# Kernel tuning notes

Hardware: AMD Instinct MI355X
Metric: run time of the kernel (lower is better)

The kernel has to match this reference:

```python
import jax, jax.numpy as jnp
import numpy as np

# static module config (matches init_kwargs)
DIM = 128
HEADS = 8
DW, HW, WW = 5, 7, 7  # depth/height/width window


def _neighbor_indices(D, H, W):
    """Flat circular-neighborhood indices, shape (P, n) with P=D*H*W, n=DW*HW*WW."""
    od = np.arange(DW) - (DW - 1) // 2
    oh = np.arange(HW) - (HW - 1) // 2
    ow = np.arange(WW) - (WW - 1) // 2
    dd = (np.arange(D)[:, None] + od[None, :]) % D   # (D, DW)
    hh = (np.arange(H)[:, None] + oh[None, :]) % H   # (H, HW)
    ww = (np.arange(W)[:, None] + ow[None, :]) % W   # (W, WW)
    idx = (dd[:, None, None, :, None, None] * (H * W)
           + hh[None, :, None, None, :, None] * W
           + ww[None, None, :, None, None, :])        # (D,H,W,DW,HW,WW)
    return jnp.asarray(idx.reshape(D * H * W, DW * HW * WW), dtype=jnp.int32)


def setup_inputs() -> dict:
    key = jax.random.key(0)
    k1, k2, k3, k4, k5 = jax.random.split(key, 5)
    B, D, H, W, C = 1, 5, 24, 48, DIM
    w_scale = 1.0 / np.sqrt(C)  # keep attention logits in a sane range
    return {
        "x": jax.random.normal(k1, (B, D, H, W, C), dtype=jnp.float32),
        "qkv_w": jax.random.normal(k2, (3 * C, C), dtype=jnp.float32) * w_scale,
        "qkv_b": jax.random.normal(k3, (3 * C,), dtype=jnp.float32) * 0.01,
        "proj_w": jax.random.normal(k4, (C, C), dtype=jnp.float32) * w_scale,
        "proj_b": jax.random.normal(k5, (C,), dtype=jnp.float32) * 0.01,
    }


def reference(x, qkv_w, qkv_b, proj_w, proj_b):
    B, D, H, W, C = x.shape
    P = D * H * W
    n = DW * HW * WW
    hd = C // HEADS
    scale = hd ** -0.5
    idx = _neighbor_indices(D, H, W)                      # (P, n) int32, static

    xf = x.reshape(B, P, C)
    qkv = xf @ qkv_w.T + qkv_b                            # (B, P, 3C)
    q, k, v = jnp.split(qkv, 3, axis=-1)

    q = q.reshape(B, P, HEADS, hd)                        # center-pixel query
    k_g = k[:, idx].reshape(B, P, n, HEADS, hd)           # gathered circular neighborhood
    v_g = v[:, idx].reshape(B, P, n, HEADS, hd)

    scores = jnp.einsum('bphd,bpnhd->bhpn', q, k_g) * scale
    attn = jax.nn.softmax(scores, axis=-1)                # softmax over 245 neighbors
    out = jnp.einsum('bhpn,bpnhd->bphd', attn, v_g).reshape(B, P, C)
    out = out @ proj_w.T + proj_b
    return out.reshape(B, D, H, W, C)
```

## Files before the change

kernel.cpp:

```cpp
#include <hip/hip_runtime.h>
#include <hip/hip_bf16.h>
#include <cstddef>

#define DIMC   128
#define NHEADS 8
#define HDIM   16
#define DD     5
#define HH     24
#define WW_    48
#define NPOS   (DD * HH * WW_)
#define SCALE  0.25f

typedef short  bf16x8 __attribute__((ext_vector_type(8)));
typedef float  f32x4  __attribute__((ext_vector_type(4)));

__device__ __forceinline__ unsigned short f2bf(float f) {
    unsigned u = __float_as_uint(f);
    u = (u + 0x7FFFu + ((u >> 16) & 1u)) >> 16;
    return (unsigned short)u;
}
__device__ __forceinline__ float bf2f(unsigned short s) {
    return __uint_as_float(((unsigned)s) << 16);
}

__global__ __launch_bounds__(256) void prep_kernel(
    const float* __restrict__ x,
    const float* __restrict__ wq,
    const float* __restrict__ wp,
    unsigned short* __restrict__ Axq,
    unsigned short* __restrict__ Bxq,
    unsigned short* __restrict__ Bxp)
{
    const int i = blockIdx.x * 256 + threadIdx.x;
    const bool isA = (i < 184320);
    const float* src; unsigned short* dst; int rel;
    if (isA)             { src = x;  dst = Axq; rel = i; }
    else if (i < 196608) { src = wq; dst = Bxq; rel = i - 184320; }
    else                 { src = wp; dst = Bxp; rel = i - 196608; }
    const int row = rel >> 5;
    const int c4  = rel & 31;
    const float4 v = *(const float4*)(src + (size_t)row * 128 + c4 * 4);
    ushort4 hi, lo;
    hi.x = f2bf(v.x); hi.y = f2bf(v.y); hi.z = f2bf(v.z); hi.w = f2bf(v.w);
    lo.x = f2bf(v.x - bf2f(hi.x));
    lo.y = f2bf(v.y - bf2f(hi.y));
    lo.z = f2bf(v.z - bf2f(hi.z));
    lo.w = f2bf(v.w - bf2f(hi.w));
    unsigned short* p = dst + (size_t)row * 384 + c4 * 4;
    if (isA) {
        *(ushort4*)(p)       = hi;
        *(ushort4*)(p + 128) = lo;
        *(ushort4*)(p + 256) = hi;
    } else {
        *(ushort4*)(p)       = hi;
        *(ushort4*)(p + 128) = hi;
        *(ushort4*)(p + 256) = lo;
    }
}

template <int MI, int EPI>
__global__ __launch_bounds__(256, 3) void gemm_mfma_kernel(
    const unsigned short* __restrict__ Ax,
    const unsigned short* __restrict__ Bx,
    const float* __restrict__ bias,
    float* __restrict__ C, int ldc,
    unsigned short* __restrict__ Qhl,
    unsigned short* __restrict__ Kbf,
    unsigned short* __restrict__ Vbf)
{
    __shared__ __align__(16) unsigned short Bs[64][392];

    const int tid = threadIdx.x;
    const int bn  = blockIdx.x * 64;
    const int bm  = blockIdx.y * 64 * MI;

    for (int i = tid; i < 64 * 48; i += 256) {
        const int r = i / 48, s = i % 48;
        *(ulonglong2*)(&Bs[r][s * 8]) =
            *(const ulonglong2*)(Bx + (size_t)(bn + r) * 384 + s * 8);
    }
    __syncthreads();

    const int w    = tid >> 6;
    const int lane = tid & 63;
    const int ln   = lane & 15;
    const int quad = lane >> 4;

    f32x4 acc[MI][4] = {};
    const unsigned short* arow[MI];
    #pragma unroll
    for (int mi = 0; mi < MI; ++mi)
        arow[mi] = Ax + (size_t)(bm + w * 16 * MI + mi * 16 + ln) * 384 + quad * 8;

    #pragma unroll
    for (int kc = 0; kc < 12; ++kc) {
        bf16x8 a[MI];
        #pragma unroll
        for (int mi = 0; mi < MI; ++mi) a[mi] = *(const bf16x8*)(arow[mi] + kc * 32);
        #pragma unroll
        for (int nt = 0; nt < 4; ++nt) {
            const bf16x8 b = *(const bf16x8*)(&Bs[nt * 16 + ln][kc * 32 + quad * 8]);
            #pragma unroll
            for (int mi = 0; mi < MI; ++mi)
                acc[mi][nt] = __builtin_amdgcn_mfma_f32_16x16x32_bf16(a[mi], b, acc[mi][nt], 0, 0, 0);
        }
    }

    #pragma unroll
    for (int mi = 0; mi < MI; ++mi)
        #pragma unroll
        for (int nt = 0; nt < 4; ++nt) {
            const int col = bn + nt * 16 + ln;
            const float bv = bias[col];
            #pragma unroll
            for (int r = 0; r < 4; ++r) {
                const int row = bm + w * 16 * MI + mi * 16 + quad * 4 + r;
                const float val = acc[mi][nt][r] + bv;
                if (EPI == 0) {
                    C[(size_t)row * ldc + col] = val;
                } else {
                    if (col < 128) {
                        const int h = col >> 4, ci = col & 15;
                        const unsigned short hi = f2bf(val);
                        Qhl[(size_t)row * 256 + h * 32 + ci]      = hi;
                        Qhl[(size_t)row * 256 + h * 32 + 16 + ci] = f2bf(val - bf2f(hi));
                    } else if (col < 256) {
                        Kbf[(size_t)row * 128 + (col - 128)] = f2bf(val);
                    } else {
                        Vbf[(size_t)row * 128 + (col - 256)] = f2bf(val);
                    }
                }
            }
        }
}

__global__ __launch_bounds__(256, 3) void attn_kernel(
    const unsigned short* __restrict__ Qhl,
    const unsigned short* __restrict__ Kbf,
    const unsigned short* __restrict__ Vbf,
    unsigned short* __restrict__ Ap)
{
    __shared__ __align__(16) char smem[34560];
    unsigned short (*Vt)[520] = (unsigned short(*)[520])smem;
    unsigned short (*Qb)[40]  = (unsigned short(*)[40])(smem + 16640);
    unsigned short* PwBase    = (unsigned short*)(smem + 23040);
    float* red_l              = (float*)(smem + 33280);
    float* redO               = (float*)smem;

    const int tile = blockIdx.x;
    const int h    = blockIdx.y;
    const int ty0  = (tile / 12) * 4;
    const int tx0  = (tile % 12) * 4;
    const int tid  = threadIdx.x;

    for (int i = tid; i < 1024; i += 256) {
        const int u = i >> 1, half = i & 1;
        if (u < 500) {
            const int dp = u / 100;
            const int rr = u - dp * 100;
            const int yy = rr / 10;
            const int xx = rr - yy * 10;
            int y = ty0 - 3 + yy; if (y < 0) y += HH;  if (y >= HH) y -= HH;
            int x = tx0 - 3 + xx; if (x < 0) x += WW_; if (x >= WW_) x -= WW_;
            const int g = (dp * HH + y) * WW_ + x;
            const bf16x8 v = *(const bf16x8*)(Vbf + (size_t)g * 128 + h * 16 + half * 8);
            #pragma unroll
            for (int c = 0; c < 8; ++c) Vt[half * 8 + c][u] = (unsigned short)v[c];
        } else {
            #pragma unroll
            for (int c = 0; c < 8; ++c) Vt[half * 8 + c][u] = 0;
        }
    }
    for (int i = tid; i < 320; i += 256) {
        const int p = i >> 2, seg = i & 3;
        const int d = p >> 4, s = p & 15;
        const int sy = s >> 2, sx = s & 3;
        const int g = (d * HH + ty0 + sy) * WW_ + tx0 + sx;
        *(bf16x8*)(&Qb[p][seg * 8]) = *(const bf16x8*)(Qhl + (size_t)g * 256 + h * 32 + seg * 8);
    }
    __syncthreads();

    const int w    = tid >> 6;
    const int lane = tid & 63;
    const int ln   = lane & 15;
    const int quad = lane >> 4;
    const int sy   = ln >> 2, sx = ln & 3;

    unsigned short* Pw = PwBase + w * 1280;

    bf16x8 qf[5];
    #pragma unroll
    for (int mt = 0; mt < 5; ++mt)
        qf[mt] = *(const bf16x8*)(&Qb[mt * 16 + ln][quad * 8]);

    f32x4 Ow[5] = {};
    float lsum[5] = {};

    for (int chunk = 0; chunk < 4; ++chunk) {
        const int u0 = (w * 4 + chunk) * 32;

        int rowa, rowb;
        {
            const int ua = u0 + ln      < 500 ? u0 + ln      : 499;
            const int ub = u0 + 16 + ln < 500 ? u0 + 16 + ln : 499;
            int dp = ua / 100, rr = ua - dp * 100, yy = rr / 10, xx = rr - yy * 10;
            int y = ty0 - 3 + yy; if (y < 0) y += HH;  if (y >= HH) y -= HH;
            int x = tx0 - 3 + xx; if (x < 0) x += WW_; if (x >= WW_) x -= WW_;
            rowa = (dp * HH + y) * WW_ + x;
            dp = ub / 100; rr = ub - dp * 100; yy = rr / 10; xx = rr - yy * 10;
            y = ty0 - 3 + yy; if (y < 0) y += HH;  if (y >= HH) y -= HH;
            x = tx0 - 3 + xx; if (x < 0) x += WW_; if (x >= WW_) x -= WW_;
            rowb = (dp * HH + y) * WW_ + x;
        }
        const bf16x8 ka = *(const bf16x8*)(Kbf + (size_t)rowa * 128 + h * 16 + (quad & 1) * 8);
        const bf16x8 kb = *(const bf16x8*)(Kbf + (size_t)rowb * 128 + h * 16 + (quad & 1) * 8);

        bool msk[2][4];
        #pragma unroll
        for (int b = 0; b < 2; ++b)
            #pragma unroll
            for (int r = 0; r < 4; ++r) {
                const int u = u0 + 16 * b + 4 * quad + r;
                const int rr = u % 100;
                const int uy = rr / 10, ux = rr - uy * 10;
                msk[b][r] = (u < 500) && ((unsigned)(uy - sy) <= 6u)
                                      && ((unsigned)(ux - sx) <= 6u);
            }

        const bf16x8 vf = *(const bf16x8*)(&Vt[ln][u0 + quad * 8]);

        #pragma unroll
        for (int mt = 0; mt < 5; ++mt) {
            f32x4 s0 = __builtin_amdgcn_mfma_f32_16x16x32_bf16(
                ka, qf[mt], (f32x4){0.f, 0.f, 0.f, 0.f}, 0, 0, 0);
            f32x4 s1 = __builtin_amdgcn_mfma_f32_16x16x32_bf16(
                kb, qf[mt], (f32x4){0.f, 0.f, 0.f, 0.f}, 0, 0, 0);

            unsigned short* pw = Pw + (mt & 1) * 640 + ln * 40;
            #pragma unroll
            for (int b = 0; b < 2; ++b) {
                const f32x4 s = b ? s1 : s0;
                unsigned short e[4];
                #pragma unroll
                for (int r = 0; r < 4; ++r) {
                    const float ev = msk[b][r] ? __expf(fmaf(s[r], SCALE, -8.0f)) : 0.f;
                    e[r] = f2bf(ev);
                    lsum[mt] += bf2f(e[r]);
                }
                *(unsigned*)(pw + 16 * b + 4 * quad)     = (unsigned)e[0] | ((unsigned)e[1] << 16);
                *(unsigned*)(pw + 16 * b + 4 * quad + 2) = (unsigned)e[2] | ((unsigned)e[3] << 16);
            }
            const bf16x8 pf = *(const bf16x8*)(Pw + (mt & 1) * 640 + ln * 40 + quad * 8);
            Ow[mt] = __builtin_amdgcn_mfma_f32_16x16x32_bf16(vf, pf, Ow[mt], 0, 0, 0);
        }
    }

    #pragma unroll
    for (int mt = 0; mt < 5; ++mt) {
        lsum[mt] += __shfl_xor(lsum[mt], 16);
        lsum[mt] += __shfl_xor(lsum[mt], 32);
    }

    __syncthreads();

    if (quad == 0) {
        #pragma unroll
        for (int mt = 0; mt < 5; ++mt) red_l[w * 80 + mt * 16 + ln] = lsum[mt];
    }
    #pragma unroll
    for (int mt = 0; mt < 5; ++mt)
        #pragma unroll
        for (int r = 0; r < 4; ++r)
            redO[(size_t)((w * 5 + mt) * 16 + quad * 4 + r) * 16 + ln] = Ow[mt][r];
    __syncthreads();

    for (int i = tid; i < 1280; i += 256) {
        const int m = i >> 4, c = i & 15;
        const int mt = m >> 4, mloc = m & 15;
        float o = 0.f, l = 0.f;
        #pragma unroll
        for (int w4 = 0; w4 < 4; ++w4) {
            o += redO[(size_t)((w4 * 5 + mt) * 16 + c) * 16 + mloc];
            l += red_l[w4 * 80 + m];
        }
        const float val = o / l;
        const int qsy = (mloc >> 2), qsx = mloc & 3;
        const size_t g = (size_t)((mt * HH + ty0 + qsy) * WW_ + (tx0 + qsx));
        const unsigned short hi = f2bf(val);
        const unsigned short lo = f2bf(val - bf2f(hi));
        unsigned short* row = Ap + g * 384 + h * HDIM + c;
        row[0]   = hi;
        row[128] = lo;
        row[256] = hi;
    }
}

extern "C" void kernel_launch(void* const* d_in, const int* in_sizes, int n_in,
                              void* d_out, int out_size, void* d_ws, size_t ws_size,
                              hipStream_t stream)
{
    const float* x      = (const float*)d_in[0];
    const float* qkv_w  = (const float*)d_in[1];
    const float* qkv_b  = (const float*)d_in[2];
    const float* proj_w = (const float*)d_in[3];
    const float* proj_b = (const float*)d_in[4];
    float* out = (float*)d_out;

    char* ws = (char*)d_ws;
    unsigned short* Axq = (unsigned short*)ws;  ws += (size_t)NPOS * 384 * 2;
    unsigned short* Ap  = (unsigned short*)ws;  ws += (size_t)NPOS * 384 * 2;
    unsigned short* Bxq = (unsigned short*)ws;  ws += (size_t)384 * 384 * 2;
    unsigned short* Bxp = (unsigned short*)ws;  ws += (size_t)128 * 384 * 2;
    unsigned short* Qhl = (unsigned short*)ws;  ws += (size_t)NPOS * 256 * 2;
    unsigned short* Kbf = (unsigned short*)ws;  ws += (size_t)NPOS * 128 * 2;
    unsigned short* Vbf = (unsigned short*)ws;  ws += (size_t)NPOS * 128 * 2;

    prep_kernel<<<784, 256, 0, stream>>>(x, qkv_w, proj_w, Axq, Bxq, Bxp);

    {
        dim3 grid(384 / 64, NPOS / 128);
        gemm_mfma_kernel<2, 1><<<grid, 256, 0, stream>>>(
            Axq, Bxq, qkv_b, nullptr, 0, Qhl, Kbf, Vbf);
    }
    {
        dim3 grid(72, NHEADS);
        attn_kernel<<<grid, 256, 0, stream>>>(Qhl, Kbf, Vbf, Ap);
    }
    {
        dim3 grid(DIMC / 64, NPOS / 64);
        gemm_mfma_kernel<1, 0><<<grid, 256, 0, stream>>>(
            Ap, Bxp, proj_b, out, DIMC, nullptr, nullptr, nullptr);
    }
}
```

Baseline: 107.4 us.

## Repartition attention work so each wave owns one depth slice's queries

The attention kernel now uses 320 threads (5 waves), and each wave owns the 16 queries of one depth slice and loops over all 500 neighbor keys. Previously the 4 waves split the keys and held all 5 query tiles, so partial outputs had to be reduced across waves in shared memory. The change removes that reduction and its barriers and moves neighbor row indices and per-query mask bitmasks into shared-memory tables. It also switches to exp2 with folded constants, truncates to bf16 instead of rounding, and packs two V rows per shared store. The trade-off is fewer blocks per CU and more serial MFMA work per wave.

```diff
diff --git a/kernel.cpp b/kernel.cpp
--- a/kernel.cpp
+++ b/kernel.cpp
@@ -134,18 +134,17 @@
         }
 }
 
-__global__ __launch_bounds__(256, 3) void attn_kernel(
+__global__ __launch_bounds__(320, 2) void attn_kernel(
     const unsigned short* __restrict__ Qhl,
     const unsigned short* __restrict__ Kbf,
     const unsigned short* __restrict__ Vbf,
     unsigned short* __restrict__ Ap)
 {
-    __shared__ __align__(16) char smem[34560];
-    unsigned short (*Vt)[520] = (unsigned short(*)[520])smem;
-    unsigned short (*Qb)[40]  = (unsigned short(*)[40])(smem + 16640);
-    unsigned short* PwBase    = (unsigned short*)(smem + 23040);
-    float* red_l              = (float*)(smem + 33280);
-    float* redO               = (float*)smem;
+    __shared__ __align__(16) unsigned short Vt[16][520];
+    __shared__ __align__(16) unsigned short Qb[80][40];
+    __shared__ __align__(16) unsigned short Pw[5][2][16][40];
+    __shared__ unsigned short Mb2[16][34];
+    __shared__ int RowL[512];
 
     const int tile = blockIdx.x;
     const int h    = blockIdx.y;
@@ -153,26 +152,55 @@
     const int tx0  = (tile % 12) * 4;
     const int tid  = threadIdx.x;
 
-    for (int i = tid; i < 1024; i += 256) {
-        const int u = i >> 1, half = i & 1;
-        if (u < 500) {
-            const int dp = u / 100;
-            const int rr = u - dp * 100;
-            const int yy = rr / 10;
-            const int xx = rr - yy * 10;
-            int y = ty0 - 3 + yy; if (y < 0) y += HH;  if (y >= HH) y -= HH;
-            int x = tx0 - 3 + xx; if (x < 0) x += WW_; if (x >= WW_) x -= WW_;
-            const int g = (dp * HH + y) * WW_ + x;
-            const bf16x8 v = *(const bf16x8*)(Vbf + (size_t)g * 128 + h * 16 + half * 8);
-            #pragma unroll
-            for (int c = 0; c < 8; ++c) Vt[half * 8 + c][u] = (unsigned short)v[c];
-        } else {
-            #pragma unroll
-            for (int c = 0; c < 8; ++c) Vt[half * 8 + c][u] = 0;
-        }
-    }
-    for (int i = tid; i < 320; i += 256) {
-        const int p = i >> 2, seg = i & 3;
+    for (int u = tid; u < 512; u += 320) {
+        const int uc = u < 500 ? u : 499;
+        const int dp = uc / 100, rr = uc % 100;
+        const int uy = rr / 10,  ux = rr % 10;
+        int y = ty0 - 3 + uy; if (y < 0) y += HH;  if (y >= HH) y -= HH;
+        int x = tx0 - 3 + ux; if (x < 0) x += WW_; if (x >= WW_) x -= WW_;
+        RowL[u] = (dp * HH + y) * WW_ + x;
+    }
+    for (int i = tid; i < 512; i += 320) {
+        const int t = i >> 4, ln = i & 15;
+        const int sy = ln >> 2, sx = ln & 3;
+        unsigned bits = 0;
+        #pragma unroll
+        for (int b = 0; b < 16; ++b) {
+            const int u = t * 16 + b;
+            const int rr = u % 100;
+            const int uy = rr / 10, ux = rr % 10;
+            if (u < 500 && (unsigned)(uy - sy) <= 6u && (unsigned)(ux - sx) <= 6u)
+                bits |= 1u << b;
+        }
+        Mb2[ln][t] = (unsigned short)bits;
+    }
+    for (int i = tid; i < 256; i += 320) {
+        const int u0 = i * 2;
+        unsigned short va[16], vb[16];
+        #pragma unroll
+        for (int c = 0; c < 16; ++c) { va[c] = 0; vb[c] = 0; }
+        #pragma unroll
+        for (int half = 0; half < 2; ++half) {
+            const int u = u0 + half;
+            if (u < 500) {
+                const int dp = u / 100, rr = u % 100;
+                const int uy = rr / 10,  ux = rr % 10;
+                int y = ty0 - 3 + uy; if (y < 0) y += HH;  if (y >= HH) y -= HH;
+                int x = tx0 - 3 + ux; if (x < 0) x += WW_; if (x >= WW_) x -= WW_;
+                const int g = (dp * HH + y) * WW_ + x;
+                const bf16x8 p0 = *(const bf16x8*)(Vbf + (size_t)g * 128 + h * 16);
+                const bf16x8 p1 = *(const bf16x8*)(Vbf + (size_t)g * 128 + h * 16 + 8);
+                unsigned short* dst = half ? vb : va;
+                #pragma unroll
+                for (int c = 0; c < 8; ++c) { dst[c] = (unsigned short)p0[c]; dst[8 + c] = (unsigned short)p1[c]; }
+            }
+        }
+        #pragma unroll
+        for (int c = 0; c < 16; ++c)
+            *(unsigned*)(&Vt[c][u0]) = (unsigned)va[c] | ((unsigned)vb[c] << 16);
+    }
+    {
+        const int p = tid >> 2, seg = tid & 3;
         const int d = p >> 4, s = p & 15;
         const int sy = s >> 2, sx = s & 3;
         const int g = (d * HH + ty0 + sy) * WW_ + tx0 + sx;
@@ -184,115 +212,69 @@
     const int lane = tid & 63;
     const int ln   = lane & 15;
     const int quad = lane >> 4;
-    const int sy   = ln >> 2, sx = ln & 3;
-
-    unsigned short* Pw = PwBase + w * 1280;
-
-    bf16x8 qf[5];
-    #pragma unroll
-    for (int mt = 0; mt < 5; ++mt)
-        qf[mt] = *(const bf16x8*)(&Qb[mt * 16 + ln][quad * 8]);
-
-    f32x4 Ow[5] = {};
-    float lsum[5] = {};
-
-    for (int chunk = 0; chunk < 4; ++chunk) {
-        const int u0 = (w * 4 + chunk) * 32;
-
-        int rowa, rowb;
-        {
-            const int ua = u0 + ln      < 500 ? u0 + ln      : 499;
-            const int ub = u0 + 16 + ln < 500 ? u0 + 16 + ln : 499;
-            int dp = ua / 100, rr = ua - dp * 100, yy = rr / 10, xx = rr - yy * 10;
-            int y = ty0 - 3 + yy; if (y < 0) y += HH;  if (y >= HH) y -= HH;
-            int x = tx0 - 3 + xx; if (x < 0) x += WW_; if (x >= WW_) x -= WW_;
-            rowa = (dp * HH + y) * WW_ + x;
-            dp = ub / 100; rr = ub - dp * 100; yy = rr / 10; xx = rr - yy * 10;
-            y = ty0 - 3 + yy; if (y < 0) y += HH;  if (y >= HH) y -= HH;
-            x = tx0 - 3 + xx; if (x < 0) x += WW_; if (x >= WW_) x -= WW_;
-            rowb = (dp * HH + y) * WW_ + x;
-        }
-        const bf16x8 ka = *(const bf16x8*)(Kbf + (size_t)rowa * 128 + h * 16 + (quad & 1) * 8);
-        const bf16x8 kb = *(const bf16x8*)(Kbf + (size_t)rowb * 128 + h * 16 + (quad & 1) * 8);
-
-        bool msk[2][4];
-        #pragma unroll
-        for (int b = 0; b < 2; ++b)
+
+    const bf16x8 qf = *(const bf16x8*)(&Qb[w * 16 + ln][quad * 8]);
+    f32x4 Ow = {0.f, 0.f, 0.f, 0.f};
+    float lsum = 0.f;
+
+    const float C1 = SCALE * 1.44269504f;
+    const float C0 = -11.5415603f;
+
+    #pragma unroll 4
+    for (int c = 0; c < 16; ++c) {
+        const int u0 = c * 32;
+        const int g0 = RowL[u0 + ln];
+        const int g1 = RowL[u0 + 16 + ln];
+        const bf16x8 k0 = *(const bf16x8*)(Kbf + (size_t)g0 * 128 + h * 16 + (quad & 1) * 8);
+        const bf16x8 k1 = *(const bf16x8*)(Kbf + (size_t)g1 * 128 + h * 16 + (quad & 1) * 8);
+        const unsigned mb = *(const unsigned*)(&Mb2[ln][2 * c]);
+        const unsigned m0 = (mb >> (quad * 4)) & 0xF;
+        const unsigned m1 = (mb >> (16 + quad * 4)) & 0xF;
+
+        f32x4 s0 = __builtin_amdgcn_mfma_f32_16x16x32_bf16(k0, qf, (f32x4){0.f,0.f,0.f,0.f}, 0, 0, 0);
+        f32x4 s1 = __builtin_amdgcn_mfma_f32_16x16x32_bf16(k1, qf, (f32x4){0.f,0.f,0.f,0.f}, 0, 0, 0);
+
+        unsigned short* pw = &Pw[w][c & 1][ln][0];
+        #pragma unroll
+        for (int t = 0; t < 2; ++t) {
+            const f32x4 s = t ? s1 : s0;
+            const unsigned m = t ? m1 : m0;
+            unsigned eu[4];
             #pragma unroll
             for (int r = 0; r < 4; ++r) {
-                const int u = u0 + 16 * b + 4 * quad + r;
-                const int rr = u % 100;
-                const int uy = rr / 10, ux = rr - uy * 10;
-                msk[b][r] = (u < 500) && ((unsigned)(uy - sy) <= 6u)
-                                      && ((unsigned)(ux - sx) <= 6u);
+                const float arg = ((m >> r) & 1u) ? fmaf(s[r], C1, C0) : -100.f;
+                const unsigned trunc = __float_as_uint(exp2f(arg)) & 0xFFFF0000u;
+                eu[r] = trunc;
+                lsum += __uint_as_float(trunc);
             }
+            unsigned* dst = (unsigned*)(pw + t * 16 + quad * 4);
+            dst[0] = (eu[0] >> 16) | eu[1];
+            dst[1] = (eu[2] >> 16) | eu[3];
+        }
 
         const bf16x8 vf = *(const bf16x8*)(&Vt[ln][u0 + quad * 8]);
-
-        #pragma unroll
-        for (int mt = 0; mt < 5; ++mt) {
-            f32x4 s0 = __builtin_amdgcn_mfma_f32_16x16x32_bf16(
-                ka, qf[mt], (f32x4){0.f, 0.f, 0.f, 0.f}, 0, 0, 0);
-            f32x4 s1 = __builtin_amdgcn_mfma_f32_16x16x32_bf16(
-                kb, qf[mt], (f32x4){0.f, 0.f, 0.f, 0.f}, 0, 0, 0);
-
-            unsigned short* pw = Pw + (mt & 1) * 640 + ln * 40;
-            #pragma unroll
-            for (int b = 0; b < 2; ++b) {
-                const f32x4 s = b ? s1 : s0;
-                unsigned short e[4];
-                #pragma unroll
-                for (int r = 0; r < 4; ++r) {
-                    const float ev = msk[b][r] ? __expf(fmaf(s[r], SCALE, -8.0f)) : 0.f;
-                    e[r] = f2bf(ev);
-                    lsum[mt] += bf2f(e[r]);
-                }
-                *(unsigned*)(pw + 16 * b + 4 * quad)     = (unsigned)e[0] | ((unsigned)e[1] << 16);
-                *(unsigned*)(pw + 16 * b + 4 * quad + 2) = (unsigned)e[2] | ((unsigned)e[3] << 16);
-            }
-            const bf16x8 pf = *(const bf16x8*)(Pw + (mt & 1) * 640 + ln * 40 + quad * 8);
-            Ow[mt] = __builtin_amdgcn_mfma_f32_16x16x32_bf16(vf, pf, Ow[mt], 0, 0, 0);
-        }
-    }
-
-    #pragma unroll
-    for (int mt = 0; mt < 5; ++mt) {
-        lsum[mt] += __shfl_xor(lsum[mt], 16);
-        lsum[mt] += __shfl_xor(lsum[mt], 32);
-    }
-
-    __syncthreads();
-
-    if (quad == 0) {
-        #pragma unroll
-        for (int mt = 0; mt < 5; ++mt) red_l[w * 80 + mt * 16 + ln] = lsum[mt];
-    }
-    #pragma unroll
-    for (int mt = 0; mt < 5; ++mt)
-        #pragma unroll
-        for (int r = 0; r < 4; ++r)
-            redO[(size_t)((w * 5 + mt) * 16 + quad * 4 + r) * 16 + ln] = Ow[mt][r];
-    __syncthreads();
-
-    for (int i = tid; i < 1280; i += 256) {
-        const int m = i >> 4, c = i & 15;
-        const int mt = m >> 4, mloc = m & 15;
-        float o = 0.f, l = 0.f;
-        #pragma unroll
-        for (int w4 = 0; w4 < 4; ++w4) {
-            o += redO[(size_t)((w4 * 5 + mt) * 16 + c) * 16 + mloc];
-            l += red_l[w4 * 80 + m];
-        }
-        const float val = o / l;
-        const int qsy = (mloc >> 2), qsx = mloc & 3;
-        const size_t g = (size_t)((mt * HH + ty0 + qsy) * WW_ + (tx0 + qsx));
-        const unsigned short hi = f2bf(val);
-        const unsigned short lo = f2bf(val - bf2f(hi));
-        unsigned short* row = Ap + g * 384 + h * HDIM + c;
-        row[0]   = hi;
-        row[128] = lo;
-        row[256] = hi;
-    }
+        const bf16x8 pf = *(const bf16x8*)(&Pw[w][c & 1][ln][quad * 8]);
+        Ow = __builtin_amdgcn_mfma_f32_16x16x32_bf16(vf, pf, Ow, 0, 0, 0);
+    }
+
+    lsum += __shfl_xor(lsum, 16);
+    lsum += __shfl_xor(lsum, 32);
+    const float inv = 1.0f / lsum;
+
+    const int sy = ln >> 2, sx = ln & 3;
+    const size_t g = (size_t)((w * HH + ty0 + sy) * WW_ + (tx0 + sx));
+    ushort4 hi4, lo4;
+    {
+        float v0 = Ow[0] * inv, v1 = Ow[1] * inv, v2 = Ow[2] * inv, v3 = Ow[3] * inv;
+        hi4.x = f2bf(v0); lo4.x = f2bf(v0 - bf2f(hi4.x));
+        hi4.y = f2bf(v1); lo4.y = f2bf(v1 - bf2f(hi4.y));
+        hi4.z = f2bf(v2); lo4.z = f2bf(v2 - bf2f(hi4.z));
+        hi4.w = f2bf(v3); lo4.w = f2bf(v3 - bf2f(hi4.w));
+    }
+    unsigned short* row = Ap + g * 384 + h * HDIM + quad * 4;
+    *(ushort4*)(row)       = hi4;
+    *(ushort4*)(row + 128) = lo4;
+    *(ushort4*)(row + 256) = hi4;
 }
 
 extern "C" void kernel_launch(void* const* d_in, const int* in_sizes, int n_in,
@@ -324,7 +306,7 @@
     }
     {
         dim3 grid(72, NHEADS);
-        attn_kernel<<<grid, 256, 0, stream>>>(Qhl, Kbf, Vbf, Ap);
+        attn_kernel<<<grid, 320, 0, stream>>>(Qhl, Kbf, Vbf, Ap);
     }
     {
         dim3 grid(DIMC / 64, NPOS / 64);
```

Measured after the change: 110.4 us. 2.8% more time.

## Fuse bf16 split conversion into GEMM kernels and drop prep pass

Applied to the files above, without the earlier changes.

Removes the separate prep kernel that expanded x and the weights into 3x-wide hi/lo/hi bf16 buffers. The QKV GEMM now reads fp32 x and weights directly, splits them into hi/lo in registers and shared memory, and issues three MFMAs per k-step instead of streaming a tripled K dimension. The attention output buffer shrinks from 384 to 256 columns, and the projection GEMM uses smaller 128-thread blocks over 32 rows. This cuts one launch and the global traffic of the expanded operands, in exchange for redundant weight conversion in every block and less per-block M reuse.

```diff
diff --git a/kernel.cpp b/kernel.cpp
--- a/kernel.cpp
+++ b/kernel.cpp
@@ -23,61 +23,31 @@
     return __uint_as_float(((unsigned)s) << 16);
 }
 
-__global__ __launch_bounds__(256) void prep_kernel(
+__global__ __launch_bounds__(256, 3) void gemm_qkv_kernel(
     const float* __restrict__ x,
     const float* __restrict__ wq,
-    const float* __restrict__ wp,
-    unsigned short* __restrict__ Axq,
-    unsigned short* __restrict__ Bxq,
-    unsigned short* __restrict__ Bxp)
-{
-    const int i = blockIdx.x * 256 + threadIdx.x;
-    const bool isA = (i < 184320);
-    const float* src; unsigned short* dst; int rel;
-    if (isA)             { src = x;  dst = Axq; rel = i; }
-    else if (i < 196608) { src = wq; dst = Bxq; rel = i - 184320; }
-    else                 { src = wp; dst = Bxp; rel = i - 196608; }
-    const int row = rel >> 5;
-    const int c4  = rel & 31;
-    const float4 v = *(const float4*)(src + (size_t)row * 128 + c4 * 4);
-    ushort4 hi, lo;
-    hi.x = f2bf(v.x); hi.y = f2bf(v.y); hi.z = f2bf(v.z); hi.w = f2bf(v.w);
-    lo.x = f2bf(v.x - bf2f(hi.x));
-    lo.y = f2bf(v.y - bf2f(hi.y));
-    lo.z = f2bf(v.z - bf2f(hi.z));
-    lo.w = f2bf(v.w - bf2f(hi.w));
-    unsigned short* p = dst + (size_t)row * 384 + c4 * 4;
-    if (isA) {
-        *(ushort4*)(p)       = hi;
-        *(ushort4*)(p + 128) = lo;
-        *(ushort4*)(p + 256) = hi;
-    } else {
-        *(ushort4*)(p)       = hi;
-        *(ushort4*)(p + 128) = hi;
-        *(ushort4*)(p + 256) = lo;
-    }
-}
-
-template <int MI, int EPI>
-__global__ __launch_bounds__(256, 3) void gemm_mfma_kernel(
-    const unsigned short* __restrict__ Ax,
-    const unsigned short* __restrict__ Bx,
-    const float* __restrict__ bias,
-    float* __restrict__ C, int ldc,
+    const float* __restrict__ qkv_b,
     unsigned short* __restrict__ Qhl,
     unsigned short* __restrict__ Kbf,
     unsigned short* __restrict__ Vbf)
 {
-    __shared__ __align__(16) unsigned short Bs[64][392];
+    __shared__ __align__(16) unsigned short Bs[64][264];
 
     const int tid = threadIdx.x;
     const int bn  = blockIdx.x * 64;
-    const int bm  = blockIdx.y * 64 * MI;
-
-    for (int i = tid; i < 64 * 48; i += 256) {
-        const int r = i / 48, s = i % 48;
-        *(ulonglong2*)(&Bs[r][s * 8]) =
-            *(const ulonglong2*)(Bx + (size_t)(bn + r) * 384 + s * 8);
+    const int bm  = blockIdx.y * 64;
+
+    for (int i = tid; i < 2048; i += 256) {
+        const int r = i >> 5, c4 = (i & 31) * 4;
+        const float4 v = *(const float4*)(wq + (size_t)(bn + r) * 128 + c4);
+        ushort4 hi, lo;
+        hi.x = f2bf(v.x); hi.y = f2bf(v.y); hi.z = f2bf(v.z); hi.w = f2bf(v.w);
+        lo.x = f2bf(v.x - bf2f(hi.x));
+        lo.y = f2bf(v.y - bf2f(hi.y));
+        lo.z = f2bf(v.z - bf2f(hi.z));
+        lo.w = f2bf(v.w - bf2f(hi.w));
+        *(ushort4*)(&Bs[r][c4])       = hi;
+        *(ushort4*)(&Bs[r][128 + c4]) = lo;
     }
     __syncthreads();
 
@@ -85,53 +55,114 @@
     const int lane = tid & 63;
     const int ln   = lane & 15;
     const int quad = lane >> 4;
-
-    f32x4 acc[MI][4] = {};
-    const unsigned short* arow[MI];
-    #pragma unroll
-    for (int mi = 0; mi < MI; ++mi)
-        arow[mi] = Ax + (size_t)(bm + w * 16 * MI + mi * 16 + ln) * 384 + quad * 8;
-
-    #pragma unroll
-    for (int kc = 0; kc < 12; ++kc) {
-        bf16x8 a[MI];
-        #pragma unroll
-        for (int mi = 0; mi < MI; ++mi) a[mi] = *(const bf16x8*)(arow[mi] + kc * 32);
+    const int row  = bm + w * 16 + ln;
+    const float* ar = x + (size_t)row * 128 + quad * 8;
+
+    f32x4 acc[4] = {};
+    #pragma unroll
+    for (int kcg = 0; kcg < 4; ++kcg) {
+        const float4 xa = *(const float4*)(ar + kcg * 32);
+        const float4 xb = *(const float4*)(ar + kcg * 32 + 4);
+        bf16x8 ahi, alo;
+        {
+            const float vv[8] = {xa.x, xa.y, xa.z, xa.w, xb.x, xb.y, xb.z, xb.w};
+            #pragma unroll
+            for (int j = 0; j < 8; ++j) {
+                const unsigned short hh = f2bf(vv[j]);
+                ahi[j] = (short)hh;
+                alo[j] = (short)f2bf(vv[j] - bf2f(hh));
+            }
+        }
         #pragma unroll
         for (int nt = 0; nt < 4; ++nt) {
-            const bf16x8 b = *(const bf16x8*)(&Bs[nt * 16 + ln][kc * 32 + quad * 8]);
-            #pragma unroll
-            for (int mi = 0; mi < MI; ++mi)
-                acc[mi][nt] = __builtin_amdgcn_mfma_f32_16x16x32_bf16(a[mi], b, acc[mi][nt], 0, 0, 0);
-        }
-    }
-
-    #pragma unroll
-    for (int mi = 0; mi < MI; ++mi)
+            const bf16x8 bhi = *(const bf16x8*)(&Bs[nt * 16 + ln][kcg * 32 + quad * 8]);
+            const bf16x8 blo = *(const bf16x8*)(&Bs[nt * 16 + ln][128 + kcg * 32 + quad * 8]);
+            acc[nt] = __builtin_amdgcn_mfma_f32_16x16x32_bf16(ahi, bhi, acc[nt], 0, 0, 0);
+            acc[nt] = __builtin_amdgcn_mfma_f32_16x16x32_bf16(alo, bhi, acc[nt], 0, 0, 0);
+            acc[nt] = __builtin_amdgcn_mfma_f32_16x16x32_bf16(ahi, blo, acc[nt], 0, 0, 0);
+        }
+    }
+
+    #pragma unroll
+    for (int nt = 0; nt < 4; ++nt) {
+        const int col = bn + nt * 16 + ln;
+        const float bv = qkv_b[col];
+        #pragma unroll
+        for (int r = 0; r < 4; ++r) {
+            const int orow = bm + w * 16 + quad * 4 + r;
+            const float val = acc[nt][r] + bv;
+            if (col < 128) {
+                const int h = col >> 4, ci = col & 15;
+                const unsigned short hi = f2bf(val);
+                Qhl[(size_t)orow * 256 + h * 32 + ci]      = hi;
+                Qhl[(size_t)orow * 256 + h * 32 + 16 + ci] = f2bf(val - bf2f(hi));
+            } else if (col < 256) {
+                Kbf[(size_t)orow * 128 + (col - 128)] = f2bf(val);
+            } else {
+                Vbf[(size_t)orow * 128 + (col - 256)] = f2bf(val);
+            }
+        }
+    }
+}
+
+__global__ __launch_bounds__(128, 2) void gemm_proj_kernel(
+    const unsigned short* __restrict__ Ap,
+    const float* __restrict__ wp,
+    const float* __restrict__ proj_b,
+    float* __restrict__ out)
+{
+    __shared__ __align__(16) unsigned short Bs[64][264];
+
+    const int tid = threadIdx.x;
+    const int bn  = blockIdx.x * 64;
+    const int bm  = blockIdx.y * 32;
+
+    for (int i = tid; i < 2048; i += 128) {
+        const int r = i >> 5, c4 = (i & 31) * 4;
+        const float4 v = *(const float4*)(wp + (size_t)(bn + r) * 128 + c4);
+        ushort4 hi, lo;
+        hi.x = f2bf(v.x); hi.y = f2bf(v.y); hi.z = f2bf(v.z); hi.w = f2bf(v.w);
+        lo.x = f2bf(v.x - bf2f(hi.x));
+        lo.y = f2bf(v.y - bf2f(hi.y));
+        lo.z = f2bf(v.z - bf2f(hi.z));
+        lo.w = f2bf(v.w - bf2f(hi.w));
+        *(ushort4*)(&Bs[r][c4])       = hi;
+        *(ushort4*)(&Bs[r][128 + c4]) = lo;
+    }
+    __syncthreads();
+
+    const int w    = tid >> 6;
+    const int lane = tid & 63;
+    const int ln   = lane & 15;
+    const int quad = lane >> 4;
+    const int row  = bm + w * 16 + ln;
+    const unsigned short* ar = Ap + (size_t)row * 256 + quad * 8;
+
+    f32x4 acc[4] = {};
+    #pragma unroll
+    for (int kcg = 0; kcg < 4; ++kcg) {
+        const bf16x8 ahi = *(const bf16x8*)(ar + kcg * 32);
+        const bf16x8 alo = *(const bf16x8*)(ar + 128 + kcg * 32);
         #pragma unroll
         for (int nt = 0; nt < 4; ++nt) {
-            const int col = bn + nt * 16 + ln;
-            const float bv = bias[col];
-            #pragma unroll
-            for (int r = 0; r < 4; ++r) {
-                const int row = bm + w * 16 * MI + mi * 16 + quad * 4 + r;
-                const float val = acc[mi][nt][r] + bv;
-                if (EPI == 0) {
-                    C[(size_t)row * ldc + col] = val;
-                } else {
-                    if (col < 128) {
-                        const int h = col >> 4, ci = col & 15;
-                        const unsigned short hi = f2bf(val);
-                        Qhl[(size_t)row * 256 + h * 32 + ci]      = hi;
-                        Qhl[(size_t)row * 256 + h * 32 + 16 + ci] = f2bf(val - bf2f(hi));
-                    } else if (col < 256) {
-                        Kbf[(size_t)row * 128 + (col - 128)] = f2bf(val);
-                    } else {
-                        Vbf[(size_t)row * 128 + (col - 256)] = f2bf(val);
-                    }
-                }
-            }
-        }
+            const bf16x8 bhi = *(const bf16x8*)(&Bs[nt * 16 + ln][kcg * 32 + quad * 8]);
+            const bf16x8 blo = *(const bf16x8*)(&Bs[nt * 16 + ln][128 + kcg * 32 + quad * 8]);
+            acc[nt] = __builtin_amdgcn_mfma_f32_16x16x32_bf16(ahi, bhi, acc[nt], 0, 0, 0);
+            acc[nt] = __builtin_amdgcn_mfma_f32_16x16x32_bf16(alo, bhi, acc[nt], 0, 0, 0);
+            acc[nt] = __builtin_amdgcn_mfma_f32_16x16x32_bf16(ahi, blo, acc[nt], 0, 0, 0);
+        }
+    }
+
+    #pragma unroll
+    for (int nt = 0; nt < 4; ++nt) {
+        const int col = bn + nt * 16 + ln;
+        const float bv = proj_b[col];
+        #pragma unroll
+        for (int r = 0; r < 4; ++r) {
+            const int orow = bm + w * 16 + quad * 4 + r;
+            out[(size_t)orow * 128 + col] = acc[nt][r] + bv;
+        }
+    }
 }
 
 __global__ __launch_bounds__(256, 3) void attn_kernel(
@@ -265,7 +296,8 @@
 
     if (quad == 0) {
         #pragma unroll
-        for (int mt = 0; mt < 5; ++mt) red_l[w * 80 + mt * 16 + ln] = lsum[mt];
+        for (int mt = 0; mt < 5; ++mt)
+            red_l[w * 80 + mt * 16 + ln] = lsum[mt];
     }
     #pragma unroll
     for (int mt = 0; mt < 5; ++mt)
@@ -288,10 +320,9 @@
         const size_t g = (size_t)((mt * HH + ty0 + qsy) * WW_ + (tx0 + qsx));
         const unsigned short hi = f2bf(val);
         const unsigned short lo = f2bf(val - bf2f(hi));
-        unsigned short* row = Ap + g * 384 + h * HDIM + c;
+        unsigned short* row = Ap + g * 256 + h * HDIM + c;
         row[0]   = hi;
         row[128] = lo;
-        row[256] = hi;
     }
 }
 
@@ -307,28 +338,21 @@
     float* out = (float*)d_out;
 
     char* ws = (char*)d_ws;
-    unsigned short* Axq = (unsigned short*)ws;  ws += (size_t)NPOS * 384 * 2;
-    unsigned short* Ap  = (unsigned short*)ws;  ws += (size_t)NPOS * 384 * 2;
-    unsigned short* Bxq = (unsigned short*)ws;  ws += (size_t)384 * 384 * 2;
-    unsigned short* Bxp = (unsigned short*)ws;  ws += (size_t)128 * 384 * 2;
+    unsigned short* Ap  = (unsigned short*)ws;  ws += (size_t)NPOS * 256 * 2;
     unsigned short* Qhl = (unsigned short*)ws;  ws += (size_t)NPOS * 256 * 2;
     unsigned short* Kbf = (unsigned short*)ws;  ws += (size_t)NPOS * 128 * 2;
     unsigned short* Vbf = (unsigned short*)ws;  ws += (size_t)NPOS * 128 * 2;
 
-    prep_kernel<<<784, 256, 0, stream>>>(x, qkv_w, proj_w, Axq, Bxq, Bxp);
-
     {
-        dim3 grid(384 / 64, NPOS / 128);
-        gemm_mfma_kernel<2, 1><<<grid, 256, 0, stream>>>(
-            Axq, Bxq, qkv_b, nullptr, 0, Qhl, Kbf, Vbf);
+        dim3 grid(384 / 64, NPOS / 64);
+        gemm_qkv_kernel<<<grid, 256, 0, stream>>>(x, qkv_w, qkv_b, Qhl, Kbf, Vbf);
     }
     {
         dim3 grid(72, NHEADS);
         attn_kernel<<<grid, 256, 0, stream>>>(Qhl, Kbf, Vbf, Ap);
     }
     {
-        dim3 grid(DIMC / 64, NPOS / 64);
-        gemm_mfma_kernel<1, 0><<<grid, 256, 0, stream>>>(
-            Ap, Bxp, proj_b, out, DIMC, nullptr, nullptr, nullptr);
-    }
-}
+        dim3 grid(DIMC / 64, NPOS / 32);
+        gemm_proj_kernel<<<grid, 128, 0, stream>>>(Ap, proj_w, proj_b, out);
+    }
+}
```

Measured after the change: 99.85 us. 7.0% less time.
